# Kernel optimization log

Hardware: AMD Instinct MI355X
Metric: run time of the kernel (lower is better)

Reference implementation:

```python
import jax, jax.numpy as jnp
import numpy as np

N_HEADS = 16
N_EMBED = 1024
HEAD_SIZE = 64


def setup_inputs() -> dict:
    key = jax.random.key(0)
    ks = jax.random.split(key, 6)
    B, T, C = 2, 2048, N_EMBED
    x = jax.random.normal(ks[0], (B, T, C), dtype=jnp.float32)
    s = 1.0 / np.sqrt(C)
    Wq = jax.random.normal(ks[1], (N_HEADS, C, HEAD_SIZE), dtype=jnp.float32) * s
    Wk = jax.random.normal(ks[2], (N_HEADS, C, HEAD_SIZE), dtype=jnp.float32) * s
    Wv = jax.random.normal(ks[3], (N_HEADS, C, HEAD_SIZE), dtype=jnp.float32) * s
    Wo = jax.random.normal(ks[4], (C, C), dtype=jnp.float32) * s
    bo = jax.random.normal(ks[5], (C,), dtype=jnp.float32) * 0.01
    return {"x": x, "Wq": Wq, "Wk": Wk, "Wv": Wv, "Wo": Wo, "bo": bo}


def reference(x, Wq, Wk, Wv, Wo, bo):
    B, T, C = x.shape
    # per-head projections: [B, H, T, D]
    q = jnp.einsum('btc,hcd->bhtd', x, Wq)
    k = jnp.einsum('btc,hcd->bhtd', x, Wk)
    v = jnp.einsum('btc,hcd->bhtd', x, Wv)
    # NOTE: original scales by n_embed**0.5 (C), not head_size**0.5
    scores = jnp.einsum('bhtd,bhsd->bhts', q, k) / jnp.sqrt(jnp.float32(C))
    causal = jnp.tril(jnp.ones((T, T), dtype=bool))
    scores = jnp.where(causal, scores, -jnp.inf)
    wei = jax.nn.softmax(scores, axis=-1)
    out = jnp.einsum('bhts,bhsd->bhtd', wei, v)  # [B, H, T, D]
    out = out.transpose(0, 2, 1, 3).reshape(B, T, C)  # concat heads
    return out @ Wo.T + bo
```

## Files before the change

kernel.cpp:

```cpp
#include <hip/hip_runtime.h>


#define Bsz 2
#define Tsz 2048
#define Cdim 1024
#define Hn 16
#define Dh 64

typedef short bf16x8 __attribute__((ext_vector_type(8)));
typedef float f32x4 __attribute__((ext_vector_type(4)));
typedef unsigned short u16;

#define MFMA(a, b, c) __builtin_amdgcn_mfma_f32_16x16x32_bf16(a, b, c, 0, 0, 0)
#define NEGINF (-__builtin_inff())
#define EXP2(x) __builtin_amdgcn_exp2f(x)

#define GLD16(g, l)                                                            \
  __builtin_amdgcn_global_load_lds((const __attribute__((address_space(1))) void*)(g), \
                                   (__attribute__((address_space(3))) void*)(l), 16, 0, 0)

__device__ __forceinline__ u16 f2bf(float f) {
  unsigned u = __builtin_bit_cast(unsigned, f);
  unsigned r = 0x7fffu + ((u >> 16) & 1u);
  return (u16)((u + r) >> 16);
}

__device__ __forceinline__ unsigned cvtpk(float lo, float hi) {
  unsigned r;
  asm("v_cvt_pk_bf16_f32 %0, %1, %2" : "=v"(r) : "v"(lo), "v"(hi));
  return r;
}

__global__ __launch_bounds__(256) void k_cast_xw(const float* __restrict__ x,
                                                 u16* __restrict__ xb, int n4x,
                                                 const float* __restrict__ wo,
                                                 u16* __restrict__ wob, int n4w) {
  int i = blockIdx.x * 256 + threadIdx.x;
  const float* s;
  u16* d;
  if (i < n4x) {
    s = x; d = xb;
  } else {
    i -= n4x;
    if (i >= n4w) return;
    s = wo; d = wob;
  }
  float4 v = reinterpret_cast<const float4*>(s)[i];
  ushort4 o;
  o.x = f2bf(v.x); o.y = f2bf(v.y); o.z = f2bf(v.z); o.w = f2bf(v.w);
  reinterpret_cast<ushort4*>(d)[i] = o;
}

__global__ __launch_bounds__(256) void k_cast_w(const float* __restrict__ Wq,
                                                const float* __restrict__ Wk,
                                                const float* __restrict__ Wv,
                                                u16* __restrict__ wt) {
  __shared__ u16 tile[64][68];
  const int mh = blockIdx.y;
  const int m = mh >> 4, h = mh & 15;
  const float* src = (m == 0 ? Wq : m == 1 ? Wk : Wv) + (size_t)h * Cdim * Dh;
  const int c0 = blockIdx.x * 64;
  const int tid = threadIdx.x;
  const int cc = tid >> 4, d4 = (tid & 15) * 4;
#pragma unroll
  for (int i = 0; i < 4; ++i) {
    int c = i * 16 + cc;
    float4 v = *(const float4*)(src + (size_t)(c0 + c) * Dh + d4);
    tile[d4 + 0][c] = f2bf(v.x);
    tile[d4 + 1][c] = f2bf(v.y);
    tile[d4 + 2][c] = f2bf(v.z);
    tile[d4 + 3][c] = f2bf(v.w);
  }
  __syncthreads();
  const int c4 = (tid & 15) * 4, dd = tid >> 4;
#pragma unroll
  for (int i = 0; i < 4; ++i) {
    int d = i * 16 + dd;
    ushort4 o;
    o.x = tile[d][c4]; o.y = tile[d][c4 + 1];
    o.z = tile[d][c4 + 2]; o.w = tile[d][c4 + 3];
    *(ushort4*)(wt + (size_t)(mh * 64 + d) * Cdim + c0 + c4) = o;
  }
}

__global__ __launch_bounds__(256) void k_gemm_qkv(const u16* __restrict__ xb,
                                                  const u16* __restrict__ wt,
                                                  u16* __restrict__ qb,
                                                  u16* __restrict__ kb,
                                                  u16* __restrict__ vtb) {
  __shared__ __align__(16) u16 As[3][4096], Bs[3][4096];
  const int tid = threadIdx.x, lane = tid & 63, wid = tid >> 6;
  const int cl = lane & 15, kg = lane >> 4;
  const int j = blockIdx.x & 7, mb = blockIdx.x >> 3;
  const int bx = (j & 1) * 12 + (mb % 12);
  const int by = (j >> 1) * 8 + (mb / 12);
  const int row0 = by * 128, col0 = bx * 128;
  const int wrow = (wid >> 1) * 64, wcol = (wid & 1) * 64;
  f32x4 acc[4][4] = {};
  const int csrc = ((lane & 3) ^ ((lane >> 3) & 3)) * 8;
  const u16* a_src = xb + (size_t)(row0 + 32 * wid + (lane >> 2)) * Cdim + csrc;
  const u16* b_src = wt + (size_t)(col0 + 32 * wid + (lane >> 2)) * Cdim + csrc;

  auto stage = [&](int buf, int ke) {
    u16* Ad = &As[buf][1024 * wid];
    u16* Bd = &Bs[buf][1024 * wid];
    GLD16(a_src + ke, Ad);
    GLD16(a_src + 16 * Cdim + ke, Ad + 512);
    GLD16(b_src + ke, Bd);
    GLD16(b_src + 16 * Cdim + ke, Bd + 512);
  };

  const int rdswz = (kg ^ ((cl >> 1) & 3)) * 8;

  stage(0, 0);
  stage(1, 32);
  stage(2, 64);
  for (int kk = 0; kk < 32; ++kk) {
    if (kk < 30)
      asm volatile("s_waitcnt vmcnt(8)" ::: "memory");
    else if (kk == 30)
      asm volatile("s_waitcnt vmcnt(4)" ::: "memory");
    else
      asm volatile("s_waitcnt vmcnt(0)" ::: "memory");
    __builtin_amdgcn_s_barrier();
    const int cur = kk % 3;
    const u16* ar = &As[cur][(wrow + cl) * 32 + rdswz];
    const u16* br = &Bs[cur][(wcol + cl) * 32 + rdswz];
    bf16x8 af[4], bfr[4];
#pragma unroll
    for (int mi = 0; mi < 4; ++mi) af[mi] = *(const bf16x8*)(ar + mi * 512);
#pragma unroll
    for (int ni = 0; ni < 4; ++ni) bfr[ni] = *(const bf16x8*)(br + ni * 512);
#pragma unroll
    for (int mi = 0; mi < 4; ++mi)
#pragma unroll
      for (int ni = 0; ni < 4; ++ni)
        acc[mi][ni] = MFMA(af[mi], bfr[ni], acc[mi][ni]);
    __builtin_amdgcn_s_barrier();
    if (kk + 3 < 32) stage(cur, (kk + 3) * 32);
  }
#pragma unroll
  for (int mi = 0; mi < 4; ++mi) {
#pragma unroll
    for (int ni = 0; ni < 4; ++ni) {
      int n = col0 + wcol + ni * 16 + cl;
      int m = n >> 10, h = (n >> 6) & 15, d = n & 63;
#pragma unroll
      for (int j2 = 0; j2 < 4; ++j2) {
        int r = row0 + wrow + mi * 16 + kg * 4 + j2;
        int b = r >> 11, t = r & 2047;
        float av = acc[mi][ni][j2];
        if (m == 0) av *= 0.04508422f;
        u16 v = f2bf(av);
        size_t bh = (size_t)(b * Hn + h);
        if (m == 0)
          qb[(bh * Tsz + t) * Dh + d] = v;
        else if (m == 1)
          kb[(bh * Tsz + t) * Dh + d] = v;
        else
          vtb[(bh * Dh + d) * Tsz + t] = v;
      }
    }
  }
}

__global__ __launch_bounds__(256, 4) void k_attn(const u16* __restrict__ qb,
                                                 const u16* __restrict__ kb,
                                                 const u16* __restrict__ vtb,
                                                 u16* __restrict__ ob) {
  __shared__ __align__(16) u16 KV[2][8192];
  __shared__ __align__(16) u16 Plds[4][1024];
  const int lane = threadIdx.x & 63, wid = threadIdx.x >> 6;
  const int cl = lane & 15, kg = lane >> 4;
  const int s = blockIdx.x >> 3;
  const int t = 31 - (s >> 2);
  const int p = (blockIdx.x & 7) + 8 * (s & 3);
  const int h = p & 15, b = p >> 4;
  const int qr = t * 64 + wid * 16;
  const size_t bh = (size_t)(b * Hn + h);
  const u16* Qp = qb + bh * Tsz * Dh;
  const u16* Kp = kb + bh * Tsz * Dh;
  const u16* Vp = vtb + bh * Dh * Tsz;

  const u16* pk_src[2];
  const u16* pv_src[2];
#pragma unroll
  for (int c = 0; c < 2; ++c) {
    int lo = c * 4096 + wid * 1024 + lane * 16;
    int r = lo >> 7, cb = lo & 127;
    int cbs = cb ^ ((r & 7) << 4);
    pk_src[c] = Kp + r * Dh + (cbs >> 1);
    pv_src[c] = Vp + (size_t)r * Tsz + (cbs >> 1);
  }

  auto stage = [&](int buf, int kt) {
    GLD16(pk_src[0] + kt * 4096, &KV[buf][(wid * 1024) >> 1]);
    GLD16(pk_src[1] + kt * 4096, &KV[buf][(4096 + wid * 1024) >> 1]);
    GLD16(pv_src[0] + kt * 64, &KV[buf][(8192 + wid * 1024) >> 1]);
    GLD16(pv_src[1] + kt * 64, &KV[buf][(12288 + wid * 1024) >> 1]);
  };

  bf16x8 qa0 = *(const bf16x8*)(Qp + (size_t)(qr + cl) * Dh + kg * 8);
  bf16x8 qa1 = *(const bf16x8*)(Qp + (size_t)(qr + cl) * Dh + 32 + kg * 8);

  f32x4 o[4] = {};
  float m = NEGINF, l = 0.f;

  char* pb = (char*)&Plds[wid][0];
  const int rdoff0 = ((cl << 7) + (kg << 4)) ^ ((cl & 7) << 4);
  const int rdoff1 = ((cl << 7) + 64 + (kg << 4)) ^ ((cl & 7) << 4);
  const int rowoff = wid * 16;
  const int swz0 = (kg * 16) ^ ((cl & 7) << 4);
  const int swz1 = (kg * 16 + 64) ^ ((cl & 7) << 4);

  stage(0, 0);
  __syncthreads();
  int cur = 0;
  for (int kt = 0; kt <= t; ++kt) {
    if (kt < t) stage(cur ^ 1, kt + 1);
    char* kvb = (char*)&KV[cur][0];
    bf16x8 ka[8];
#pragma unroll
    for (int nt = 0; nt < 4; ++nt) {
      int rbase = (nt * 16 + cl) << 7;
      ka[nt * 2] = *(const bf16x8*)(kvb + rbase + swz0);
      ka[nt * 2 + 1] = *(const bf16x8*)(kvb + rbase + swz1);
    }
    f32x4 sv[4];
    __builtin_amdgcn_s_setprio(1);
#pragma unroll
    for (int nt = 0; nt < 4; ++nt) {
      f32x4 z = {};
      z = MFMA(ka[nt * 2], qa0, z);
      z = MFMA(ka[nt * 2 + 1], qa1, z);
      sv[nt] = z;
    }
    __builtin_amdgcn_s_setprio(0);
    bf16x8 vf[8];
#pragma unroll
    for (int dt = 0; dt < 4; ++dt) {
      int rbase = 8192 + ((dt * 16 + cl) << 7);
      vf[dt * 2] = *(const bf16x8*)(kvb + rbase + swz0);
      vf[dt * 2 + 1] = *(const bf16x8*)(kvb + rbase + swz1);
    }
    if (kt == t) {
#pragma unroll
      for (int nt = 0; nt < 4; ++nt)
#pragma unroll
        for (int j = 0; j < 4; ++j)
          if (nt * 16 + kg * 4 + j > rowoff + cl) sv[nt][j] = NEGINF;
    }
    float tm = fmaxf(fmaxf(fmaxf(sv[0][0], sv[0][1]), fmaxf(sv[0][2], sv[0][3])),
                     fmaxf(fmaxf(sv[1][0], sv[1][1]), fmaxf(sv[1][2], sv[1][3])));
    tm = fmaxf(tm, fmaxf(fmaxf(fmaxf(sv[2][0], sv[2][1]), fmaxf(sv[2][2], sv[2][3])),
                         fmaxf(fmaxf(sv[3][0], sv[3][1]), fmaxf(sv[3][2], sv[3][3]))));
    if (!__all(tm <= m + 8.0f)) {
      tm = fmaxf(tm, __shfl_xor(tm, 16));
      tm = fmaxf(tm, __shfl_xor(tm, 32));
      float mnew = fmaxf(m, tm);
      float corr = EXP2(m - mnew);
      m = mnew;
      l *= corr;
      float c0 = __shfl(corr, kg * 4 + 0);
      float c1 = __shfl(corr, kg * 4 + 1);
      float c2 = __shfl(corr, kg * 4 + 2);
      float c3 = __shfl(corr, kg * 4 + 3);
#pragma unroll
      for (int dt = 0; dt < 4; ++dt) {
        o[dt][0] *= c0; o[dt][1] *= c1; o[dt][2] *= c2; o[dt][3] *= c3;
      }
    }
    float rs = 0.f;
#pragma unroll
    for (int nt = 0; nt < 4; ++nt)
#pragma unroll
      for (int j = 0; j < 4; ++j) {
        float pv = EXP2(sv[nt][j] - m);
        sv[nt][j] = pv;
        rs += pv;
      }
    l += rs;
#pragma unroll
    for (int nt = 0; nt < 4; ++nt) {
      uint2 pk;
      pk.x = cvtpk(sv[nt][0], sv[nt][1]);
      pk.y = cvtpk(sv[nt][2], sv[nt][3]);
      int waddr = ((cl << 7) + (nt << 5) + (kg << 3)) ^ ((cl & 7) << 4);
      *(uint2*)(pb + waddr) = pk;
    }
    bf16x8 pa0 = *(const bf16x8*)(pb + rdoff0);
    bf16x8 pa1 = *(const bf16x8*)(pb + rdoff1);
    __builtin_amdgcn_s_setprio(1);
#pragma unroll
    for (int dt = 0; dt < 4; ++dt) {
      o[dt] = MFMA(pa0, vf[dt * 2], o[dt]);
      o[dt] = MFMA(pa1, vf[dt * 2 + 1], o[dt]);
    }
    __builtin_amdgcn_s_setprio(0);
    __syncthreads();
    cur ^= 1;
  }

  l += __shfl_xor(l, 16);
  l += __shfl_xor(l, 32);
  float i0 = 1.f / __shfl(l, kg * 4 + 0), i1 = 1.f / __shfl(l, kg * 4 + 1);
  float i2 = 1.f / __shfl(l, kg * 4 + 2), i3 = 1.f / __shfl(l, kg * 4 + 3);
  float inv[4] = {i0, i1, i2, i3};
#pragma unroll
  for (int dt = 0; dt < 4; ++dt)
#pragma unroll
    for (int j = 0; j < 4; ++j) {
      int tr = qr + kg * 4 + j;
      ob[(size_t)(b * Tsz + tr) * Cdim + h * Dh + dt * 16 + cl] = f2bf(o[dt][j] * inv[j]);
    }
}

__global__ __launch_bounds__(256) void k_gemm_out(const u16* __restrict__ ob,
                                                  const u16* __restrict__ wob,
                                                  const float* __restrict__ bo,
                                                  float* __restrict__ out) {
  __shared__ __align__(16) u16 As[3][4096], Bs[3][2048];
  const int tid = threadIdx.x, lane = tid & 63, wid = tid >> 6;
  const int cl = lane & 15, kg = lane >> 4;
  const int j = blockIdx.x & 7, mb = blockIdx.x >> 3;
  const int bx = (j & 1) * 8 + (mb % 8);
  const int by = (j >> 1) * 8 + (mb / 8);
  const int row0 = by * 128, col0 = bx * 64;
  const int wrow = (wid >> 1) * 64, wcol = (wid & 1) * 32;
  f32x4 acc[4][2] = {};
  const int csrc = ((lane & 3) ^ ((lane >> 3) & 3)) * 8;
  const u16* a_src = ob + (size_t)(row0 + 32 * wid + (lane >> 2)) * Cdim + csrc;
  const u16* b_src = wob + (size_t)(col0 + 16 * wid + (lane >> 2)) * Cdim + csrc;

  auto stage = [&](int buf, int ke) {
    u16* Ad = &As[buf][1024 * wid];
    u16* Bd = &Bs[buf][512 * wid];
    GLD16(a_src + ke, Ad);
    GLD16(a_src + 16 * Cdim + ke, Ad + 512);
    GLD16(b_src + ke, Bd);
  };

  const int rdswz = (kg ^ ((cl >> 1) & 3)) * 8;

  stage(0, 0);
  stage(1, 32);
  stage(2, 64);
  for (int kk = 0; kk < 32; ++kk) {
    if (kk < 30)
      asm volatile("s_waitcnt vmcnt(6)" ::: "memory");
    else if (kk == 30)
      asm volatile("s_waitcnt vmcnt(3)" ::: "memory");
    else
      asm volatile("s_waitcnt vmcnt(0)" ::: "memory");
    __builtin_amdgcn_s_barrier();
    const int cur = kk % 3;
    const u16* ar = &As[cur][(wrow + cl) * 32 + rdswz];
    const u16* br = &Bs[cur][(wcol + cl) * 32 + rdswz];
    bf16x8 af[4], bfr[2];
#pragma unroll
    for (int mi = 0; mi < 4; ++mi) af[mi] = *(const bf16x8*)(ar + mi * 512);
#pragma unroll
    for (int ni = 0; ni < 2; ++ni) bfr[ni] = *(const bf16x8*)(br + ni * 512);
#pragma unroll
    for (int mi = 0; mi < 4; ++mi)
#pragma unroll
      for (int ni = 0; ni < 2; ++ni)
        acc[mi][ni] = MFMA(af[mi], bfr[ni], acc[mi][ni]);
    __builtin_amdgcn_s_barrier();
    if (kk + 3 < 32) stage(cur, (kk + 3) * 32);
  }
#pragma unroll
  for (int mi = 0; mi < 4; ++mi) {
#pragma unroll
    for (int ni = 0; ni < 2; ++ni) {
      int n = col0 + wcol + ni * 16 + cl;
      float bias = bo[n];
#pragma unroll
      for (int j2 = 0; j2 < 4; ++j2) {
        int r = row0 + wrow + mi * 16 + kg * 4 + j2;
        out[(size_t)r * Cdim + n] = acc[mi][ni][j2] + bias;
      }
    }
  }
}

extern "C" void kernel_launch(void* const* d_in, const int* in_sizes, int n_in,
                              void* d_out, int out_size, void* d_ws, size_t ws_size,
                              hipStream_t stream) {
  (void)in_sizes; (void)n_in; (void)out_size; (void)ws_size;
  const float* x = (const float*)d_in[0];
  const float* Wq = (const float*)d_in[1];
  const float* Wk = (const float*)d_in[2];
  const float* Wv = (const float*)d_in[3];
  const float* Wo = (const float*)d_in[4];
  const float* bo = (const float*)d_in[5];
  float* out = (float*)d_out;
  char* ws = (char*)d_ws;
  u16* xb = (u16*)(ws);
  u16* wt = (u16*)(ws + (8u << 20));
  u16* wob = (u16*)(ws + (14u << 20));
  u16* qb = (u16*)(ws + (16u << 20));
  u16* kb = (u16*)(ws + (24u << 20));
  u16* vtb = (u16*)(ws + (32u << 20));
  u16* ob = (u16*)(ws + (40u << 20));

  const int n4x = Bsz * Tsz * Cdim / 4, n4w = Cdim * Cdim / 4;
  k_cast_xw<<<(n4x + n4w + 255) / 256, 256, 0, stream>>>(x, xb, n4x, Wo, wob, n4w);
  k_cast_w<<<dim3(16, 48), 256, 0, stream>>>(Wq, Wk, Wv, wt);
  k_gemm_qkv<<<768, 256, 0, stream>>>(xb, wt, qb, kb, vtb);
  k_attn<<<1024, 256, 0, stream>>>(qb, kb, vtb, ob);
  k_gemm_out<<<512, 256, 0, stream>>>(ob, wob, bo, out);
}
```

Baseline: 113.8 us.

## Enlarge QKV GEMM tile to 256x256 with 8 waves and split-phase pipeline

The QKV projection GEMM moves from 128x128 tiles with 4 waves to 256x256 tiles with 8 waves per block, so 192 blocks run instead of 768. Each K-step is split into two MFMA phases, and the A and B global-to-LDS loads for later stages are interleaved between them. s_setprio and sched_barrier are added to favour MFMA issue. This aims for more operand reuse per LDS byte and better overlap of loads with compute. The cost is fewer blocks than the 256 CUs, leaving some CUs idle, plus higher register and LDS pressure.

```diff
diff --git a/kernel.cpp b/kernel.cpp
--- a/kernel.cpp
+++ b/kernel.cpp
@@ -83,82 +83,102 @@
   }
 }
 
-__global__ __launch_bounds__(256) void k_gemm_qkv(const u16* __restrict__ xb,
-                                                  const u16* __restrict__ wt,
-                                                  u16* __restrict__ qb,
-                                                  u16* __restrict__ kb,
-                                                  u16* __restrict__ vtb) {
-  __shared__ __align__(16) u16 As[3][4096], Bs[3][4096];
+__global__ __launch_bounds__(512, 2) void k_gemm_qkv(const u16* __restrict__ xb,
+                                                     const u16* __restrict__ wt,
+                                                     u16* __restrict__ qb,
+                                                     u16* __restrict__ kb,
+                                                     u16* __restrict__ vtb) {
+  __shared__ __align__(16) u16 As[3][8192], Bs[3][8192];
   const int tid = threadIdx.x, lane = tid & 63, wid = tid >> 6;
   const int cl = lane & 15, kg = lane >> 4;
+  const int wm = wid >> 2, wn = wid & 3;
   const int j = blockIdx.x & 7, mb = blockIdx.x >> 3;
-  const int bx = (j & 1) * 12 + (mb % 12);
-  const int by = (j >> 1) * 8 + (mb / 12);
-  const int row0 = by * 128, col0 = bx * 128;
-  const int wrow = (wid >> 1) * 64, wcol = (wid & 1) * 64;
-  f32x4 acc[4][4] = {};
-  const int csrc = ((lane & 3) ^ ((lane >> 3) & 3)) * 8;
-  const u16* a_src = xb + (size_t)(row0 + 32 * wid + (lane >> 2)) * Cdim + csrc;
-  const u16* b_src = wt + (size_t)(col0 + 32 * wid + (lane >> 2)) * Cdim + csrc;
-
-  auto stage = [&](int buf, int ke) {
-    u16* Ad = &As[buf][1024 * wid];
-    u16* Bd = &Bs[buf][1024 * wid];
-    GLD16(a_src + ke, Ad);
-    GLD16(a_src + 16 * Cdim + ke, Ad + 512);
-    GLD16(b_src + ke, Bd);
-    GLD16(b_src + 16 * Cdim + ke, Bd + 512);
+  const int bx = (j & 1) * 6 + (mb % 6);
+  const int by = (j >> 1) * 4 + (mb / 6);
+  const int row0 = by * 256, col0 = bx * 256;
+  f32x4 acc[8][4] = {};
+  const int csrc = ((tid & 3) ^ ((tid >> 3) & 3)) * 8;
+  const int srow = tid >> 2;
+  const u16* a_src0 = xb + (size_t)(row0 + srow) * Cdim + csrc;
+  const u16* a_src1 = xb + (size_t)(row0 + 128 + srow) * Cdim + csrc;
+  const u16* b_src0 = wt + (size_t)(col0 + srow) * Cdim + csrc;
+  const u16* b_src1 = wt + (size_t)(col0 + 128 + srow) * Cdim + csrc;
+
+  auto stageA = [&](int buf, int kt) {
+    GLD16(a_src0 + kt * 32, &As[buf][wid * 512]);
+    GLD16(a_src1 + kt * 32, &As[buf][4096 + wid * 512]);
   };
-
+  auto stageB = [&](int buf, int kt) {
+    GLD16(b_src0 + kt * 32, &Bs[buf][wid * 512]);
+    GLD16(b_src1 + kt * 32, &Bs[buf][4096 + wid * 512]);
+  };
   const int rdswz = (kg ^ ((cl >> 1) & 3)) * 8;
 
-  stage(0, 0);
-  stage(1, 32);
-  stage(2, 64);
-  for (int kk = 0; kk < 32; ++kk) {
-    if (kk < 30)
-      asm volatile("s_waitcnt vmcnt(8)" ::: "memory");
-    else if (kk == 30)
+  stageA(0, 0); stageB(0, 0); stageA(1, 1); stageB(1, 1); stageB(2, 2);
+
+  for (int t = 0; t < 32; ++t) {
+    const int cur = t % 3;
+    if (t <= 29)
+      asm volatile("s_waitcnt vmcnt(6)" ::: "memory");
+    else if (t == 30)
       asm volatile("s_waitcnt vmcnt(4)" ::: "memory");
     else
       asm volatile("s_waitcnt vmcnt(0)" ::: "memory");
     __builtin_amdgcn_s_barrier();
-    const int cur = kk % 3;
-    const u16* ar = &As[cur][(wrow + cl) * 32 + rdswz];
-    const u16* br = &Bs[cur][(wcol + cl) * 32 + rdswz];
     bf16x8 af[4], bfr[4];
 #pragma unroll
-    for (int mi = 0; mi < 4; ++mi) af[mi] = *(const bf16x8*)(ar + mi * 512);
-#pragma unroll
-    for (int ni = 0; ni < 4; ++ni) bfr[ni] = *(const bf16x8*)(br + ni * 512);
-#pragma unroll
-    for (int mi = 0; mi < 4; ++mi)
-#pragma unroll
-      for (int ni = 0; ni < 4; ++ni)
-        acc[mi][ni] = MFMA(af[mi], bfr[ni], acc[mi][ni]);
-    __builtin_amdgcn_s_barrier();
-    if (kk + 3 < 32) stage(cur, (kk + 3) * 32);
-  }
-#pragma unroll
-  for (int mi = 0; mi < 4; ++mi) {
+    for (int m = 0; m < 4; ++m)
+      af[m] = *(const bf16x8*)&As[cur][(wm * 128 + m * 16 + cl) * 32 + rdswz];
+#pragma unroll
+    for (int n = 0; n < 4; ++n)
+      bfr[n] = *(const bf16x8*)&Bs[cur][(wn * 64 + n * 16 + cl) * 32 + rdswz];
+    if (t + 2 < 32) stageA((t + 2) % 3, t + 2);
+    __builtin_amdgcn_s_barrier();
+    asm volatile("s_waitcnt lgkmcnt(0)" ::: "memory");
+    __builtin_amdgcn_sched_barrier(0);
+    __builtin_amdgcn_s_setprio(1);
+#pragma unroll
+    for (int m = 0; m < 4; ++m)
+#pragma unroll
+      for (int n = 0; n < 4; ++n)
+        acc[m][n] = MFMA(af[m], bfr[n], acc[m][n]);
+    __builtin_amdgcn_s_setprio(0);
+    __builtin_amdgcn_s_barrier();
+#pragma unroll
+    for (int m = 0; m < 4; ++m)
+      af[m] = *(const bf16x8*)&As[cur][(wm * 128 + 64 + m * 16 + cl) * 32 + rdswz];
+    if (t + 3 < 32) stageB((t + 3) % 3, t + 3);
+    __builtin_amdgcn_s_barrier();
+    asm volatile("s_waitcnt lgkmcnt(0)" ::: "memory");
+    __builtin_amdgcn_sched_barrier(0);
+    __builtin_amdgcn_s_setprio(1);
+#pragma unroll
+    for (int m = 0; m < 4; ++m)
+#pragma unroll
+      for (int n = 0; n < 4; ++n)
+        acc[4 + m][n] = MFMA(af[m], bfr[n], acc[4 + m][n]);
+    __builtin_amdgcn_s_setprio(0);
+  }
+#pragma unroll
+  for (int mi = 0; mi < 8; ++mi) {
 #pragma unroll
     for (int ni = 0; ni < 4; ++ni) {
-      int n = col0 + wcol + ni * 16 + cl;
+      int n = col0 + wn * 64 + ni * 16 + cl;
       int m = n >> 10, h = (n >> 6) & 15, d = n & 63;
 #pragma unroll
       for (int j2 = 0; j2 < 4; ++j2) {
-        int r = row0 + wrow + mi * 16 + kg * 4 + j2;
-        int b = r >> 11, t = r & 2047;
+        int r = row0 + wm * 128 + mi * 16 + kg * 4 + j2;
+        int b = r >> 11, tt = r & 2047;
         float av = acc[mi][ni][j2];
         if (m == 0) av *= 0.04508422f;
         u16 v = f2bf(av);
         size_t bh = (size_t)(b * Hn + h);
         if (m == 0)
-          qb[(bh * Tsz + t) * Dh + d] = v;
+          qb[(bh * Tsz + tt) * Dh + d] = v;
         else if (m == 1)
-          kb[(bh * Tsz + t) * Dh + d] = v;
+          kb[(bh * Tsz + tt) * Dh + d] = v;
         else
-          vtb[(bh * Dh + d) * Tsz + t] = v;
+          vtb[(bh * Dh + d) * Tsz + tt] = v;
       }
     }
   }
@@ -407,7 +427,7 @@
   const int n4x = Bsz * Tsz * Cdim / 4, n4w = Cdim * Cdim / 4;
   k_cast_xw<<<(n4x + n4w + 255) / 256, 256, 0, stream>>>(x, xb, n4x, Wo, wob, n4w);
   k_cast_w<<<dim3(16, 48), 256, 0, stream>>>(Wq, Wk, Wv, wt);
-  k_gemm_qkv<<<768, 256, 0, stream>>>(xb, wt, qb, kb, vtb);
+  k_gemm_qkv<<<192, 512, 0, stream>>>(xb, wt, qb, kb, vtb);
   k_attn<<<1024, 256, 0, stream>>>(qb, kb, vtb, ob);
   k_gemm_out<<<512, 256, 0, stream>>>(ob, wob, bo, out);
 }
```

New measurement: 127.1 us. 1.12x slower.
